# Performance work log

Measured on AMD Instinct MI355X. Metric: run time of the kernel, lower is better.

The kernel has to match this reference:

```python
import jax, jax.numpy as jnp
import numpy as np
import math

IN_F, OUT_F = 512, 512
N_HEADS, N_SPLITS = 32, 4
N = 1024
DELTA_SCALE = 0.1


def setup_inputs() -> dict:
    key = jax.random.key(0)
    k_x, k_h, k_s, k_w = jax.random.split(key, 4)
    stdv = 1.0 / math.sqrt(OUT_F)
    inputs = {
        "input": jax.random.normal(k_x, (N, IN_F), dtype=jnp.float32),
        "head_ix": jax.random.randint(k_h, (N,), 0, N_HEADS, dtype=jnp.int32),
        "split_ix": jax.random.randint(k_s, (N,), 0, N_SPLITS, dtype=jnp.int32),
        # learned parameters (EmbeddingTensor tables)
        "weight": jax.random.uniform(k_w, (N_HEADS, IN_F, OUT_F), dtype=jnp.float32,
                                     minval=-stdv, maxval=stdv),
        "delta_weight": jnp.zeros((N_HEADS * N_SPLITS, IN_F, OUT_F), dtype=jnp.float32),
        "bias": jnp.zeros((N_HEADS, OUT_F), dtype=jnp.float32),
    }
    return inputs


def reference(input, head_ix, split_ix, weight, delta_weight, bias):
    # per-sample weight: base[head] + 0.1 * delta[head * n_splits + split]
    w = weight[head_ix] + delta_weight[head_ix * N_SPLITS + split_ix] * DELTA_SCALE  # [N, in, out]
    # batched vector-matrix multiply + per-head bias
    return jnp.einsum('ab,abc->ac', input, w) + bias[head_ix]  # [N, out]
```

## Files before the change

### kernel.cpp

```cpp
#include <hip/hip_runtime.h>

#define N_SAMP   1024
#define IN_F     512
#define OUT_F    512
#define N_HEADS  32
#define N_SPLITS 4
#define DELTA_SCALE 0.1f

__device__ __forceinline__ void fma4(float4& a, float x, const float4& w) {
    a.x += x * w.x; a.y += x * w.y; a.z += x * w.z; a.w += x * w.w;
}
__device__ __forceinline__ void add4(float4& a, const float4& b) {
    a.x += b.x; a.y += b.y; a.z += b.z; a.w += b.w;
}

template <int JCOV, int KC, bool DELTA>
__device__ __forceinline__ void role_pass(
    const float* __restrict__ X, const int* __restrict__ head_ix,
    const int* __restrict__ split_ix, const float* __restrict__ Wslice,
    const float* __restrict__ bias_g, float* __restrict__ dst,
    int g, int c0, int sampleBase, float* buf, int* list, int* wsum)
{
    constexpr int NST = KC / 8;
    constexpr int NCH = IN_F / KC;
    constexpr int QW  = KC / 4;

    const int tid  = threadIdx.x;
    const int lane = tid & 63, wave = tid >> 6;
    const int ct   = tid & 31;
    const int kq   = (tid >> 5) & 1;

    int run = 0;
    for (int r = 0; r < N_SAMP / 256; ++r) {
        const int i   = r * 256 + tid;
        const int key = DELTA ? head_ix[i] * N_SPLITS + split_ix[i] : head_ix[i];
        const bool hit = (key == g);
        const unsigned long long m = __ballot(hit);
        if (lane == 0) wsum[wave] = __popcll(m);
        __syncthreads();
        int base = run;
        for (int w = 0; w < 4; ++w)
            if (w < wave) base += wsum[w];
        if (hit)
            list[base + __popcll(m & ((1ULL << lane) - 1ULL))] = i;
        run += wsum[0] + wsum[1] + wsum[2] + wsum[3];
        __syncthreads();
    }
    const int total = run;
    if (total == 0) return;

    float4 bv;
    if (!DELTA) bv = *(const float4*)(bias_g + c0 + ct * 4);

#define LDW(R, stx) {                                                        \
    const int sx_ = (stx) < NST ? (stx) : NST - 1;                           \
    const float* w_ = wp + (size_t)(sx_ * 4) * OUT_F;                        \
    R[0] = *(const float4*)(w_);                                             \
    R[1] = *(const float4*)(w_ + OUT_F);                                     \
    R[2] = *(const float4*)(w_ + 2 * OUT_F);                                 \
    R[3] = *(const float4*)(w_ + 3 * OUT_F); }
#define CONS(R, stx) {                                                       \
    _Pragma("unroll")                                                        \
    for (int j = 0; j < 16; ++j) {                                           \
        const float4 xv = *(const float4*)(xb + j * KC + (stx) * 4);         \
        fma4(acc[j], xv.x, R[0]); fma4(acc[j], xv.y, R[1]);                  \
        fma4(acc[j], xv.z, R[2]); fma4(acc[j], xv.w, R[3]); } }

    for (int s0 = 0; s0 < total; s0 += JCOV) {
        const int nc = min(total - s0, JCOV);

        float4 acc[16];
#pragma unroll
        for (int j = 0; j < 16; ++j) acc[j] = make_float4(0.f, 0.f, 0.f, 0.f);

        for (int ch = 0; ch < NCH; ++ch) {
            const int kc = ch * KC;
            __syncthreads();
            for (int i = tid; i < JCOV * QW; i += 256) {
                const int s = i / QW, q = i % QW;
                float4 v = make_float4(0.f, 0.f, 0.f, 0.f);
                if (s < nc)
                    v = *(const float4*)(X + (size_t)list[s0 + s] * IN_F + kc + q * 4);
                *(float4*)(&buf[s * KC + q * 4]) = v;
            }
            __syncthreads();

            const float* wp = Wslice + (size_t)(kc + kq * (KC / 2)) * OUT_F
                            + c0 + ct * 4;
            const float* xb = buf + (size_t)sampleBase * KC + kq * (KC / 2);

            float4 rA[4], rB[4], rC[4], rD[4];
            LDW(rA, 0); LDW(rB, 1);
            for (int st = 0; st < NST; st += 4) {
                LDW(rC, st + 2);
                CONS(rA, st);
                LDW(rD, st + 3);
                CONS(rB, st + 1);
                LDW(rA, st + 4);
                CONS(rC, st + 2);
                LDW(rB, st + 5);
                CONS(rD, st + 3);
            }
        }

#pragma unroll
        for (int j = 0; j < 16; ++j) {
            acc[j].x += __shfl_xor(acc[j].x, 32);
            acc[j].y += __shfl_xor(acc[j].y, 32);
            acc[j].z += __shfl_xor(acc[j].z, 32);
            acc[j].w += __shfl_xor(acc[j].w, 32);
        }
        if (kq == 0) {
#pragma unroll
            for (int j = 0; j < 16; ++j) {
                const int slot = sampleBase + j;
                if (slot < nc) {
                    float* op = dst + (size_t)list[s0 + slot] * OUT_F + c0 + ct * 4;
                    float4 s = acc[j];
                    if (!DELTA) add4(s, bv);
                    *(float4*)op = s;
                }
            }
        }
    }
#undef LDW
#undef CONS
}

__global__ __launch_bounds__(256, 2) void lms_fused(
    const float* __restrict__ X, const int* __restrict__ head_ix,
    const int* __restrict__ split_ix, const float* __restrict__ W,
    const float* __restrict__ D, const float* __restrict__ bias,
    float* __restrict__ out, float* __restrict__ ws)
{
    __shared__ float buf[8192];
    __shared__ int   list[N_SAMP];
    __shared__ int   wsum[4];

    const int bid  = blockIdx.x;
    const int wave = threadIdx.x >> 6;
    if (bid & 1) {
        const int id   = bid >> 1;
        const int head = id & 31, tile = id >> 5;
        role_pass<64, 128, false>(X, head_ix, split_ix,
            W + (size_t)head * IN_F * OUT_F, bias + (size_t)head * OUT_F,
            out, head, tile * 128, wave * 16, buf, list, wsum);
    } else {
        const int combo = bid >> 1;
        role_pass<16, 512, true>(X, head_ix, split_ix,
            D + (size_t)combo * IN_F * OUT_F, nullptr,
            ws, combo, wave * 128, 0, buf, list, wsum);
    }
}

__global__ __launch_bounds__(256) void combine_kernel(
    float* __restrict__ out, const float* __restrict__ ws)
{
    const int i = blockIdx.x * 256 + threadIdx.x;
    float4 o = ((float4*)out)[i];
    const float4 d = ((const float4*)ws)[i];
    o.x += DELTA_SCALE * d.x; o.y += DELTA_SCALE * d.y;
    o.z += DELTA_SCALE * d.z; o.w += DELTA_SCALE * d.w;
    ((float4*)out)[i] = o;
}

extern "C" void kernel_launch(void* const* d_in, const int* in_sizes, int n_in,
                              void* d_out, int out_size, void* d_ws, size_t ws_size,
                              hipStream_t stream) {
    const float* X        = (const float*)d_in[0];
    const int*   head_ix  = (const int*)d_in[1];
    const int*   split_ix = (const int*)d_in[2];
    const float* W        = (const float*)d_in[3];
    const float* D        = (const float*)d_in[4];
    const float* bias     = (const float*)d_in[5];
    float*       out      = (float*)d_out;
    float*       ws       = (float*)d_ws;

    lms_fused<<<256, 256, 0, stream>>>(X, head_ix, split_ix, W, D, bias, out, ws);
    combine_kernel<<<(N_SAMP * OUT_F / 4) / 256, 256, 0, stream>>>(out, ws);
}
```

Before: 285.0 us.

## Restructure fused kernel to 512-thread blocks covering full output width

```diff
diff --git a/kernel.cpp b/kernel.cpp
--- a/kernel.cpp
+++ b/kernel.cpp
@@ -14,142 +14,138 @@
     a.x += b.x; a.y += b.y; a.z += b.z; a.w += b.w;
 }
 
-template <int JCOV, int KC, bool DELTA>
-__device__ __forceinline__ void role_pass(
+template <bool DELTA, int SSTRIDE>
+__device__ __forceinline__ void role512(
     const float* __restrict__ X, const int* __restrict__ head_ix,
     const int* __restrict__ split_ix, const float* __restrict__ Wslice,
-    const float* __restrict__ bias_g, float* __restrict__ dst,
-    int g, int c0, int sampleBase, float* buf, int* list, int* wsum)
+    const float* __restrict__ bias_h, float* __restrict__ dst,
+    int g, int sampleBase, float* Xs, int* list, int* wsum)
 {
-    constexpr int NST = KC / 8;
-    constexpr int NCH = IN_F / KC;
-    constexpr int QW  = KC / 4;
-
     const int tid  = threadIdx.x;
     const int lane = tid & 63, wave = tid >> 6;
-    const int ct   = tid & 31;
-    const int kq   = (tid >> 5) & 1;
+    const int c4   = lane & 15;
+    const int p    = (lane >> 4) & 3;
+    const int cb   = wave * 64 + c4 * 4;
 
     int run = 0;
-    for (int r = 0; r < N_SAMP / 256; ++r) {
-        const int i   = r * 256 + tid;
+    for (int r = 0; r < N_SAMP / 512; ++r) {
+        const int i   = r * 512 + tid;
         const int key = DELTA ? head_ix[i] * N_SPLITS + split_ix[i] : head_ix[i];
         const bool hit = (key == g);
         const unsigned long long m = __ballot(hit);
         if (lane == 0) wsum[wave] = __popcll(m);
         __syncthreads();
-        int base = run;
-        for (int w = 0; w < 4; ++w)
+        int base = run, tot = 0;
+        for (int w = 0; w < 8; ++w) {
             if (w < wave) base += wsum[w];
+            tot += wsum[w];
+        }
         if (hit)
             list[base + __popcll(m & ((1ULL << lane) - 1ULL))] = i;
-        run += wsum[0] + wsum[1] + wsum[2] + wsum[3];
+        run += tot;
         __syncthreads();
     }
     const int total = run;
     if (total == 0) return;
 
     float4 bv;
-    if (!DELTA) bv = *(const float4*)(bias_g + c0 + ct * 4);
+    if (!DELTA) bv = *(const float4*)(bias_h + cb);
 
-#define LDW(R, stx) {                                                        \
-    const int sx_ = (stx) < NST ? (stx) : NST - 1;                           \
-    const float* w_ = wp + (size_t)(sx_ * 4) * OUT_F;                        \
-    R[0] = *(const float4*)(w_);                                             \
-    R[1] = *(const float4*)(w_ + OUT_F);                                     \
-    R[2] = *(const float4*)(w_ + 2 * OUT_F);                                 \
-    R[3] = *(const float4*)(w_ + 3 * OUT_F); }
-#define CONS(R, stx) {                                                       \
-    _Pragma("unroll")                                                        \
-    for (int j = 0; j < 16; ++j) {                                           \
-        const float4 xv = *(const float4*)(xb + j * KC + (stx) * 4);         \
-        fma4(acc[j], xv.x, R[0]); fma4(acc[j], xv.y, R[1]);                  \
-        fma4(acc[j], xv.z, R[2]); fma4(acc[j], xv.w, R[3]); } }
+    const float* wp0 = Wslice + cb;
 
-    for (int s0 = 0; s0 < total; s0 += JCOV) {
-        const int nc = min(total - s0, JCOV);
+    for (int s0 = sampleBase; s0 < total; s0 += SSTRIDE) {
+        const int nc = min(total - s0, 16);
+
+        __syncthreads();
+        for (int i = tid; i < 16 * (IN_F / 4); i += 512) {
+            const int s = i >> 7, q = i & 127;
+            float4 v = make_float4(0.f, 0.f, 0.f, 0.f);
+            if (s < nc)
+                v = *(const float4*)(X + (size_t)list[s0 + s] * IN_F + q * 4);
+            Xs[(q * 4 + 0) * 16 + s] = v.x;
+            Xs[(q * 4 + 1) * 16 + s] = v.y;
+            Xs[(q * 4 + 2) * 16 + s] = v.z;
+            Xs[(q * 4 + 3) * 16 + s] = v.w;
+        }
+        __syncthreads();
 
         float4 acc[16];
 #pragma unroll
         for (int j = 0; j < 16; ++j) acc[j] = make_float4(0.f, 0.f, 0.f, 0.f);
 
-        for (int ch = 0; ch < NCH; ++ch) {
-            const int kc = ch * KC;
-            __syncthreads();
-            for (int i = tid; i < JCOV * QW; i += 256) {
-                const int s = i / QW, q = i % QW;
-                float4 v = make_float4(0.f, 0.f, 0.f, 0.f);
-                if (s < nc)
-                    v = *(const float4*)(X + (size_t)list[s0 + s] * IN_F + kc + q * 4);
-                *(float4*)(&buf[s * KC + q * 4]) = v;
-            }
-            __syncthreads();
+        float4 wreg[8];
+#pragma unroll
+        for (int u = 0; u < 8; ++u)
+            wreg[u] = *(const float4*)(wp0 + (size_t)(4 * u + p) * OUT_F);
 
-            const float* wp = Wslice + (size_t)(kc + kq * (KC / 2)) * OUT_F
-                            + c0 + ct * 4;
-            const float* xb = buf + (size_t)sampleBase * KC + kq * (KC / 2);
-
-            float4 rA[4], rB[4], rC[4], rD[4];
-            LDW(rA, 0); LDW(rB, 1);
-            for (int st = 0; st < NST; st += 4) {
-                LDW(rC, st + 2);
-                CONS(rA, st);
-                LDW(rD, st + 3);
-                CONS(rB, st + 1);
-                LDW(rA, st + 4);
-                CONS(rC, st + 2);
-                LDW(rB, st + 5);
-                CONS(rD, st + 3);
+        for (int it0 = 0; it0 < 128; it0 += 8) {
+#pragma unroll
+            for (int u = 0; u < 8; ++u) {
+                const int it = it0 + u;
+                const int k  = 4 * it + p;
+                const float4 wv = wreg[u];
+                const float* xr = Xs + k * 16;
+#pragma unroll
+                for (int q = 0; q < 4; ++q) {
+                    const float4 xq = *(const float4*)(xr + q * 4);
+                    fma4(acc[q * 4 + 0], xq.x, wv);
+                    fma4(acc[q * 4 + 1], xq.y, wv);
+                    fma4(acc[q * 4 + 2], xq.z, wv);
+                    fma4(acc[q * 4 + 3], xq.w, wv);
+                }
+                int nit = it + 8;
+                if (nit > 127) nit = 127;
+                wreg[u] = *(const float4*)(wp0 + (size_t)(4 * nit + p) * OUT_F);
             }
         }
 
 #pragma unroll
         for (int j = 0; j < 16; ++j) {
+            acc[j].x += __shfl_xor(acc[j].x, 16);
+            acc[j].y += __shfl_xor(acc[j].y, 16);
+            acc[j].z += __shfl_xor(acc[j].z, 16);
+            acc[j].w += __shfl_xor(acc[j].w, 16);
             acc[j].x += __shfl_xor(acc[j].x, 32);
             acc[j].y += __shfl_xor(acc[j].y, 32);
             acc[j].z += __shfl_xor(acc[j].z, 32);
             acc[j].w += __shfl_xor(acc[j].w, 32);
         }
-        if (kq == 0) {
+        if (p == 0) {
 #pragma unroll
             for (int j = 0; j < 16; ++j) {
-                const int slot = sampleBase + j;
-                if (slot < nc) {
-                    float* op = dst + (size_t)list[s0 + slot] * OUT_F + c0 + ct * 4;
-                    float4 s = acc[j];
-                    if (!DELTA) add4(s, bv);
-                    *(float4*)op = s;
+                if (j < nc) {
+                    float* op = dst + (size_t)list[s0 + j] * OUT_F + cb;
+                    float4 v = acc[j];
+                    if (!DELTA) add4(v, bv);
+                    *(float4*)op = v;
                 }
             }
         }
     }
-#undef LDW
-#undef CONS
 }
 
-__global__ __launch_bounds__(256, 2) void lms_fused(
+__global__ __launch_bounds__(512, 1) void lms_fused(
     const float* __restrict__ X, const int* __restrict__ head_ix,
     const int* __restrict__ split_ix, const float* __restrict__ W,
     const float* __restrict__ D, const float* __restrict__ bias,
     float* __restrict__ out, float* __restrict__ ws)
 {
-    __shared__ float buf[8192];
+    __shared__ float Xs[IN_F * 16];
     __shared__ int   list[N_SAMP];
-    __shared__ int   wsum[4];
+    __shared__ int   wsum[8];
 
-    const int bid  = blockIdx.x;
-    const int wave = threadIdx.x >> 6;
-    if (bid & 1) {
+    const int bid = blockIdx.x;
+    if ((bid & 1) == 0) {
+        const int combo = bid >> 1;
+        role512<true, 16>(X, head_ix, split_ix,
+            D + (size_t)combo * IN_F * OUT_F, nullptr,
+            ws, combo, 0, Xs, list, wsum);
+    } else {
         const int id   = bid >> 1;
-        const int head = id & 31, tile = id >> 5;
-        role_pass<64, 128, false>(X, head_ix, split_ix,
+        const int head = id & 31, sg = id >> 5;
+        role512<false, 64>(X, head_ix, split_ix,
             W + (size_t)head * IN_F * OUT_F, bias + (size_t)head * OUT_F,
-            out, head, tile * 128, wave * 16, buf, list, wsum);
-    } else {
-        const int combo = bid >> 1;
-        role_pass<16, 512, true>(X, head_ix, split_ix,
-            D + (size_t)combo * IN_F * OUT_F, nullptr,
-            ws, combo, wave * 128, 0, buf, list, wsum);
+            out, head, sg * 16, Xs, list, wsum);
     }
 }
 
@@ -176,6 +172,6 @@
     float*       out      = (float*)d_out;
     float*       ws       = (float*)d_ws;
 
-    lms_fused<<<256, 256, 0, stream>>>(X, head_ix, split_ix, W, D, bias, out, ws);
+    lms_fused<<<256, 512, 0, stream>>>(X, head_ix, split_ix, W, D, bias, out, ws);
     combine_kernel<<<(N_SAMP * OUT_F / 4) / 256, 256, 0, stream>>>(out, ws);
 }
```

Measured after the change: 370.4 us. 30.0% more time.
